# Kernel optimization log

Hardware: AMD Instinct MI355X
Metric: run time of the kernel (lower is better)

## Reference

```python
import jax, jax.numpy as jnp
import numpy as np

B, N, M, C = 8, 76725, 32, 12  # N = 9 anchors x (80^2+40^2+20^2+10^2+5^2) for a 640x640 image, P3-P7
IMG = 640.0


def setup_inputs() -> dict:
    key = jax.random.key(0)
    ks = jax.random.split(key, 7)
    # logits biased toward prior_prob~0.01 like the head's bias init
    cls_logits = jax.random.normal(ks[0], (B, N, C), jnp.float32) - 4.0
    box_deltas = 0.1 * jax.random.normal(ks[1], (B, N, 4), jnp.float32)
    # plausible anchors: random centers in image, sizes 16..256
    a_xy = jax.random.uniform(ks[2], (N, 2), jnp.float32) * IMG
    a_wh = 16.0 + jax.random.uniform(ks[3], (N, 2), jnp.float32) * 240.0
    anchors = jnp.concatenate([a_xy - 0.5 * a_wh, a_xy + 0.5 * a_wh], axis=-1)
    # padded ground truth: M boxes per image, all valid
    g_xy = jax.random.uniform(ks[4], (B, M, 2), jnp.float32) * (IMG - 96.0)
    g_wh = 16.0 + jax.random.uniform(ks[5], (B, M, 2), jnp.float32) * 80.0
    gt_boxes = jnp.concatenate([g_xy, g_xy + g_wh], axis=-1)
    gt_labels = jax.random.randint(ks[6], (B, M), 0, C)
    gt_valid = jnp.ones((B, M), dtype=bool)
    return {"cls_logits": cls_logits, "box_deltas": box_deltas, "anchors": anchors,
            "gt_boxes": gt_boxes, "gt_labels": gt_labels, "gt_valid": gt_valid}


def _box_iou(anchors, gt_boxes):
    # anchors [N,4], gt_boxes [B,M,4] -> [B,N,M]
    ax1, ay1, ax2, ay2 = (anchors[:, i] for i in range(4))
    gx1, gy1, gx2, gy2 = (gt_boxes[..., i] for i in range(4))
    iw = jnp.clip(jnp.minimum(ax2[None, :, None], gx2[:, None, :])
                  - jnp.maximum(ax1[None, :, None], gx1[:, None, :]), 0.0)
    ih = jnp.clip(jnp.minimum(ay2[None, :, None], gy2[:, None, :])
                  - jnp.maximum(ay1[None, :, None], gy1[:, None, :]), 0.0)
    inter = iw * ih
    area_a = (ax2 - ax1) * (ay2 - ay1)            # [N]
    area_g = (gx2 - gx1) * (gy2 - gy1)            # [B,M]
    union = area_a[None, :, None] + area_g[:, None, :] - inter
    return inter / union


def _encode_boxes(anchors, matched):
    aw = anchors[:, 2] - anchors[:, 0]
    ah = anchors[:, 3] - anchors[:, 1]
    acx = anchors[:, 0] + 0.5 * aw
    acy = anchors[:, 1] + 0.5 * ah
    gw = matched[..., 2] - matched[..., 0]
    gh = matched[..., 3] - matched[..., 1]
    gcx = matched[..., 0] + 0.5 * gw
    gcy = matched[..., 1] + 0.5 * gh
    return jnp.stack([(gcx - acx) / aw, (gcy - acy) / ah,
                      jnp.log(gw / aw), jnp.log(gh / ah)], axis=-1)


def reference(cls_logits, box_deltas, anchors, gt_boxes, gt_labels, gt_valid):
    # --- anchor assignment (box_iou + max over GT) ---
    ious = _box_iou(anchors, gt_boxes)                       # [B,N,M]
    ious = jnp.where(gt_valid[:, None, :], ious, -1.0)
    iou_max = ious.max(axis=-1)                              # [B,N]
    idx = ious.argmax(axis=-1)                               # [B,N]
    pos = iou_max >= 0.5
    valid = pos | (iou_max < 0.4)                            # non-ignore anchors
    matched = jnp.take_along_axis(
        gt_boxes, jnp.broadcast_to(idx[:, :, None], (B, N, 4)), axis=1)  # [B,N,4]
    mlab = jnp.take_along_axis(gt_labels, idx, axis=1)       # [B,N]
    f32 = cls_logits.dtype
    cls_t = jax.nn.one_hot(mlab, C, dtype=f32) * pos[..., None].astype(f32)
    # --- sigmoid focal loss (alpha=0.25, gamma=2), mean over non-ignored elements ---
    p = jax.nn.sigmoid(cls_logits)
    ce = -(cls_t * jax.nn.log_sigmoid(cls_logits)
           + (1.0 - cls_t) * jax.nn.log_sigmoid(-cls_logits))
    pt = cls_t * p + (1.0 - cls_t) * (1.0 - p)
    alpha_t = cls_t * 0.25 + (1.0 - cls_t) * 0.75
    focal = alpha_t * (1.0 - pt) ** 2 * ce                   # [B,N,C]
    vw = valid.astype(f32)
    cls_loss = jnp.sum(focal * vw[..., None]) / jnp.maximum(jnp.sum(vw) * C, 1.0)
    # --- smooth L1 (beta=1) on positives, mean over selected elements ---
    box_t = _encode_boxes(anchors, matched)                  # [B,N,4]
    d = jnp.abs(box_deltas - box_t)
    sl1 = jnp.where(d < 1.0, 0.5 * d * d, d - 0.5)
    pw = pos.astype(f32)
    box_loss = jnp.sum(sl1 * pw[..., None]) / jnp.maximum(jnp.sum(pw) * 4.0, 1.0)
    return cls_loss + box_loss
```

## Files before the change

### kernel.cpp

```cpp
#include <hip/hip_runtime.h>
#include <math.h>

#define NB 8
#define NA 76725
#define NM 32
#define NC 12
#define BLK 256
#define CHX 300
#define NBLOCKS (CHX * NB)
#define WPB (BLK / 64)
#define NWAVES (NBLOCKS * WPB)


__global__ __launch_bounds__(BLK, 4) void retina_main(
    const float* __restrict__ cls_logits,
    const float* __restrict__ box_deltas,
    const float* __restrict__ anchors,
    const float* __restrict__ gt_boxes,
    const int* __restrict__ gt_labels,
    char* __restrict__ ws,
    int mode, int nslots, int sstride)
{
    const int b    = blockIdx.y;
    const int tid  = threadIdx.x;
    const int n    = blockIdx.x * BLK + tid;
    const bool live = (n < NA);
    const int nc   = live ? n : (NA - 1);

    const float4 a = ((const float4*)anchors)[nc];
    const float4* clp = (const float4*)(cls_logits + ((size_t)b * NA + nc) * NC);
    const float4 c0 = clp[0], c1 = clp[1], c2 = clp[2];
    const float4 d4 = ((const float4*)box_deltas)[(size_t)b * NA + nc];

    const float area_a = (a.z - a.x) * (a.w - a.y);
    const float4* gtb = (const float4*)gt_boxes + b * NM;

    float bi[4], bS[4]; int bx[4];
    #pragma unroll
    for (int q = 0; q < 4; ++q) {
        const int m0 = q * 8;
        {
            const float4 g = gtb[m0];
            const float iw = fmaxf(fminf(a.z, g.z) - fmaxf(a.x, g.x), 0.0f);
            const float ih = fmaxf(fminf(a.w, g.w) - fmaxf(a.y, g.y), 0.0f);
            bi[q] = iw * ih;
            bS[q] = area_a + (g.z - g.x) * (g.w - g.y);
            bx[q] = m0;
        }
        #pragma unroll
        for (int mm = 1; mm < 8; ++mm) {
            const int m = m0 + mm;
            const float4 g = gtb[m];
            const float iw = fmaxf(fminf(a.z, g.z) - fmaxf(a.x, g.x), 0.0f);
            const float ih = fmaxf(fminf(a.w, g.w) - fmaxf(a.y, g.y), 0.0f);
            const float inter = iw * ih;
            const float S     = area_a + (g.z - g.x) * (g.w - g.y);
            const bool gt = inter * bS[q] > bi[q] * S;
            bi[q] = gt ? inter : bi[q];
            bS[q] = gt ? S     : bS[q];
            bx[q] = gt ? m     : bx[q];
        }
    }
    float Bi = bi[0], BS = bS[0]; int Bx = bx[0];
    #pragma unroll
    for (int q = 1; q < 4; ++q) {
        const bool gt = bi[q] * BS > Bi * bS[q];
        Bi = gt ? bi[q] : Bi;
        BS = gt ? bS[q] : BS;
        Bx = gt ? bx[q] : Bx;
    }
    const float Bu = BS - Bi;

    const bool pos   = live && (Bi >= 0.5f * Bu);
    const bool valid = live && (pos || (Bi < 0.4f * Bu));

    const float4 g  = ((const float4*)gt_boxes)[b * NM + Bx];
    const int    ml = gt_labels[b * NM + Bx];
    const int    lab = pos ? ml : -1;

    float x[NC];
    x[0]=c0.x; x[1]=c0.y; x[2]=c0.z; x[3]=c0.w;
    x[4]=c1.x; x[5]=c1.y; x[6]=c1.z; x[7]=c1.w;
    x[8]=c2.x; x[9]=c2.y; x[10]=c2.z; x[11]=c2.w;
    float facc = 0.0f;
    #pragma unroll
    for (int c = 0; c < NC; ++c) {
        const float xx = x[c];
        const bool tgt = (c == lab);
        const float z  = tgt ? -xx : xx;
        const float e  = __expf(-fabsf(xx));
        const float t  = 1.0f + e;
        const float l  = __logf(t);
        const float u  = __builtin_amdgcn_rcpf(t);
        const float v  = e * u;
        const float q  = (z >= 0.0f) ? u : v;
        const float s  = l + fmaxf(z, 0.0f);
        const float al = tgt ? 0.25f : 0.75f;
        facc += al * (q * q) * s;
    }

    float sacc = 0.0f;
    {
        const float aw  = a.z - a.x;
        const float ah  = a.w - a.y;
        const float r_aw = __builtin_amdgcn_rcpf(aw);
        const float r_ah = __builtin_amdgcn_rcpf(ah);
        const float acx = a.x + 0.5f * aw;
        const float acy = a.y + 0.5f * ah;
        const float gw  = g.z - g.x;
        const float gh  = g.w - g.y;
        const float gcx = g.x + 0.5f * gw;
        const float gcy = g.y + 0.5f * gh;
        const float t0 = (gcx - acx) * r_aw;
        const float t1 = (gcy - acy) * r_ah;
        const float t2 = __logf(gw * r_aw);
        const float t3 = __logf(gh * r_ah);
        float d;
        d = fabsf(d4.x - t0); sacc += (d < 1.0f) ? 0.5f * d * d : d - 0.5f;
        d = fabsf(d4.y - t1); sacc += (d < 1.0f) ? 0.5f * d * d : d - 0.5f;
        d = fabsf(d4.z - t2); sacc += (d < 1.0f) ? 0.5f * d * d : d - 0.5f;
        d = fabsf(d4.w - t3); sacc += (d < 1.0f) ? 0.5f * d * d : d - 0.5f;
    }

    float4 v4 = make_float4(valid ? facc : 0.0f,
                            pos   ? sacc : 0.0f,
                            valid ? 1.0f : 0.0f,
                            pos   ? 1.0f : 0.0f);
    #pragma unroll
    for (int off = 32; off > 0; off >>= 1) {
        v4.x += __shfl_down(v4.x, off);
        v4.y += __shfl_down(v4.y, off);
        v4.z += __shfl_down(v4.z, off);
        v4.w += __shfl_down(v4.w, off);
    }
    const int lane = tid & 63;
    if (lane == 0) {
        const int wid = (b * CHX + blockIdx.x) * WPB + (tid >> 6);
        if (mode == 3) {
            ((float4*)ws)[wid] = v4;
        } else {
            double* p = (double*)(ws + (size_t)(wid & (nslots - 1)) * sstride);
            atomicAdd(&p[0], (double)v4.x);
            atomicAdd(&p[1], (double)v4.y);
            atomicAdd(&p[2], (double)v4.z);
            atomicAdd(&p[3], (double)v4.w);
        }
    }
}

__global__ __launch_bounds__(1024) void retina_finalize(
    const char* __restrict__ ws, int mode, int nslots, int sstride,
    float* __restrict__ out)
{
    const int tid = threadIdx.x;
    double fs = 0.0, ss = 0.0, vc = 0.0, pc = 0.0;
    if (mode == 3) {
        const float4* sl = (const float4*)ws;
        for (int i = tid; i < nslots; i += 1024) {
            const float4 v = sl[i];
            fs += v.x; ss += v.y; vc += v.z; pc += v.w;
        }
    } else {
        for (int i = tid; i < nslots; i += 1024) {
            const double* p = (const double*)(ws + (size_t)i * sstride);
            fs += p[0]; ss += p[1]; vc += p[2]; pc += p[3];
        }
    }
    #pragma unroll
    for (int off = 32; off > 0; off >>= 1) {
        fs += __shfl_down(fs, off);
        ss += __shfl_down(ss, off);
        vc += __shfl_down(vc, off);
        pc += __shfl_down(pc, off);
    }
    __shared__ double sred[16][4];
    const int wave = tid >> 6;
    const int lane = tid & 63;
    if (lane == 0) {
        sred[wave][0] = fs; sred[wave][1] = ss;
        sred[wave][2] = vc; sred[wave][3] = pc;
    }
    __syncthreads();
    if (tid == 0) {
        #pragma unroll
        for (int w = 1; w < 16; ++w) {
            fs += sred[w][0]; ss += sred[w][1];
            vc += sred[w][2]; pc += sred[w][3];
        }
        const double cls_loss = fs / fmax(vc * (double)NC, 1.0);
        const double box_loss = ss / fmax(pc * 4.0, 1.0);
        out[0] = (float)(cls_loss + box_loss);
    }
}

extern "C" void kernel_launch(void* const* d_in, const int* in_sizes, int n_in,
                              void* d_out, int out_size, void* d_ws, size_t ws_size,
                              hipStream_t stream) {
    const float* cls_logits = (const float*)d_in[0];
    const float* box_deltas = (const float*)d_in[1];
    const float* anchors    = (const float*)d_in[2];
    const float* gt_boxes   = (const float*)d_in[3];
    const int*   gt_labels  = (const int*)d_in[4];
    float* out = (float*)d_out;

    int mode, nslots, sstride;
    if (ws_size >= (size_t)NWAVES * 16)     { mode = 3; nslots = NWAVES; sstride = 16; }
    else if (ws_size >= (size_t)(64 * 64))  { mode = 1; nslots = 64;     sstride = 64; }
    else                                    { mode = 0; nslots = 1;      sstride = 32; }

    if (mode != 3)
        hipMemsetAsync(d_ws, 0, (size_t)nslots * sstride, stream);

    dim3 grid(CHX, NB);
    retina_main<<<grid, BLK, 0, stream>>>(
        cls_logits, box_deltas, anchors, gt_boxes, gt_labels,
        (char*)d_ws, mode, nslots, sstride);
    retina_finalize<<<1, 1024, 0, stream>>>(
        (const char*)d_ws, mode, nslots, sstride, out);
}
```

Before: 107.6 us.

## Process two anchors per thread and stage GT boxes in shared memory

Each thread now handles two anchors, which halves the grid (CHX becomes about 150) and the number of per-wave partial results and atomics. GT boxes, their areas and labels are loaded once per block into shared memory with a barrier, replacing repeated global loads and per-anchor area recomputation. The launch-bounds occupancy hint drops from 4 to 3 blocks to leave room for the extra registers, which may reduce latency hiding in this memory-bound kernel.

```diff
diff --git a/kernel.cpp b/kernel.cpp
--- a/kernel.cpp
+++ b/kernel.cpp
@@ -6,13 +6,14 @@
 #define NM 32
 #define NC 12
 #define BLK 256
-#define CHX 300
+#define APB (2 * BLK)
+#define CHX ((NA + APB - 1) / APB)
 #define NBLOCKS (CHX * NB)
 #define WPB (BLK / 64)
 #define NWAVES (NBLOCKS * WPB)
 
 
-__global__ __launch_bounds__(BLK, 4) void retina_main(
+__global__ __launch_bounds__(BLK, 3) void retina_main(
     const float* __restrict__ cls_logits,
     const float* __restrict__ box_deltas,
     const float* __restrict__ anchors,
@@ -21,111 +22,132 @@
     char* __restrict__ ws,
     int mode, int nslots, int sstride)
 {
-    const int b    = blockIdx.y;
-    const int tid  = threadIdx.x;
-    const int n    = blockIdx.x * BLK + tid;
-    const bool live = (n < NA);
-    const int nc   = live ? n : (NA - 1);
-
-    const float4 a = ((const float4*)anchors)[nc];
-    const float4* clp = (const float4*)(cls_logits + ((size_t)b * NA + nc) * NC);
-    const float4 c0 = clp[0], c1 = clp[1], c2 = clp[2];
-    const float4 d4 = ((const float4*)box_deltas)[(size_t)b * NA + nc];
-
-    const float area_a = (a.z - a.x) * (a.w - a.y);
-    const float4* gtb = (const float4*)gt_boxes + b * NM;
-
-    float bi[4], bS[4]; int bx[4];
+    __shared__ float4 s_gt[NM];
+    __shared__ float  s_area[NM];
+    __shared__ int    s_lab[NM];
+
+    const int b   = blockIdx.y;
+    const int tid = threadIdx.x;
+    const int nA  = blockIdx.x * APB + tid;
+    const int nB  = nA + BLK;
+    const bool liveA = (nA < NA);
+    const bool liveB = (nB < NA);
+    const int ncA = liveA ? nA : (NA - 1);
+    const int ncB = liveB ? nB : (NA - 1);
+
+    const float4 aA = ((const float4*)anchors)[ncA];
+    const float4 aB = ((const float4*)anchors)[ncB];
+    const float4* clpA = (const float4*)(cls_logits + ((size_t)b * NA + ncA) * NC);
+    const float4* clpB = (const float4*)(cls_logits + ((size_t)b * NA + ncB) * NC);
+    const float4 cA0 = clpA[0], cA1 = clpA[1], cA2 = clpA[2];
+    const float4 cB0 = clpB[0], cB1 = clpB[1], cB2 = clpB[2];
+    const float4 dA = ((const float4*)box_deltas)[(size_t)b * NA + ncA];
+    const float4 dB = ((const float4*)box_deltas)[(size_t)b * NA + ncB];
+
+    if (tid < NM) {
+        const float4 g = ((const float4*)gt_boxes)[b * NM + tid];
+        s_gt[tid]   = g;
+        s_area[tid] = (g.z - g.x) * (g.w - g.y);
+        s_lab[tid]  = gt_labels[b * NM + tid];
+    }
+    __syncthreads();
+
+    const float areaA = (aA.z - aA.x) * (aA.w - aA.y);
+    const float areaB = (aB.z - aB.x) * (aB.w - aB.y);
+
+#define IOU_INIT(aa, ar, g, sg, m, bi, bS, bx) do {                              \
+        const float iw_ = fmaxf(fminf((aa).z, (g).z) - fmaxf((aa).x, (g).x), 0.0f); \
+        const float ih_ = fmaxf(fminf((aa).w, (g).w) - fmaxf((aa).y, (g).y), 0.0f); \
+        (bi) = iw_ * ih_; (bS) = (ar) + (sg); (bx) = (m);                        \
+    } while (0)
+#define IOU_STEP(aa, ar, g, sg, m, bi, bS, bx) do {                              \
+        const float iw_ = fmaxf(fminf((aa).z, (g).z) - fmaxf((aa).x, (g).x), 0.0f); \
+        const float ih_ = fmaxf(fminf((aa).w, (g).w) - fmaxf((aa).y, (g).y), 0.0f); \
+        const float in_ = iw_ * ih_;                                             \
+        const float S_  = (ar) + (sg);                                           \
+        const bool gt_  = in_ * (bS) > (bi) * S_;  \
+        (bi) = gt_ ? in_ : (bi); (bS) = gt_ ? S_ : (bS); (bx) = gt_ ? (m) : (bx);\
+    } while (0)
+
+    float biA[4], bSA[4], biB[4], bSB[4];
+    int   bxA[4], bxB[4];
     #pragma unroll
     for (int q = 0; q < 4; ++q) {
         const int m0 = q * 8;
         {
-            const float4 g = gtb[m0];
-            const float iw = fmaxf(fminf(a.z, g.z) - fmaxf(a.x, g.x), 0.0f);
-            const float ih = fmaxf(fminf(a.w, g.w) - fmaxf(a.y, g.y), 0.0f);
-            bi[q] = iw * ih;
-            bS[q] = area_a + (g.z - g.x) * (g.w - g.y);
-            bx[q] = m0;
+            const float4 g = s_gt[m0]; const float sg = s_area[m0];
+            IOU_INIT(aA, areaA, g, sg, m0, biA[q], bSA[q], bxA[q]);
+            IOU_INIT(aB, areaB, g, sg, m0, biB[q], bSB[q], bxB[q]);
         }
         #pragma unroll
         for (int mm = 1; mm < 8; ++mm) {
             const int m = m0 + mm;
-            const float4 g = gtb[m];
-            const float iw = fmaxf(fminf(a.z, g.z) - fmaxf(a.x, g.x), 0.0f);
-            const float ih = fmaxf(fminf(a.w, g.w) - fmaxf(a.y, g.y), 0.0f);
-            const float inter = iw * ih;
-            const float S     = area_a + (g.z - g.x) * (g.w - g.y);
-            const bool gt = inter * bS[q] > bi[q] * S;
-            bi[q] = gt ? inter : bi[q];
-            bS[q] = gt ? S     : bS[q];
-            bx[q] = gt ? m     : bx[q];
-        }
-    }
-    float Bi = bi[0], BS = bS[0]; int Bx = bx[0];
+            const float4 g = s_gt[m]; const float sg = s_area[m];
+            IOU_STEP(aA, areaA, g, sg, m, biA[q], bSA[q], bxA[q]);
+            IOU_STEP(aB, areaB, g, sg, m, biB[q], bSB[q], bxB[q]);
+        }
+    }
+    float BiA = biA[0], BSA = bSA[0]; int BxA = bxA[0];
+    float BiB = biB[0], BSB = bSB[0]; int BxB = bxB[0];
     #pragma unroll
     for (int q = 1; q < 4; ++q) {
-        const bool gt = bi[q] * BS > Bi * bS[q];
-        Bi = gt ? bi[q] : Bi;
-        BS = gt ? bS[q] : BS;
-        Bx = gt ? bx[q] : Bx;
-    }
-    const float Bu = BS - Bi;
-
-    const bool pos   = live && (Bi >= 0.5f * Bu);
-    const bool valid = live && (pos || (Bi < 0.4f * Bu));
-
-    const float4 g  = ((const float4*)gt_boxes)[b * NM + Bx];
-    const int    ml = gt_labels[b * NM + Bx];
-    const int    lab = pos ? ml : -1;
-
-    float x[NC];
-    x[0]=c0.x; x[1]=c0.y; x[2]=c0.z; x[3]=c0.w;
-    x[4]=c1.x; x[5]=c1.y; x[6]=c1.z; x[7]=c1.w;
-    x[8]=c2.x; x[9]=c2.y; x[10]=c2.z; x[11]=c2.w;
-    float facc = 0.0f;
-    #pragma unroll
-    for (int c = 0; c < NC; ++c) {
-        const float xx = x[c];
-        const bool tgt = (c == lab);
-        const float z  = tgt ? -xx : xx;
-        const float e  = __expf(-fabsf(xx));
-        const float t  = 1.0f + e;
-        const float l  = __logf(t);
-        const float u  = __builtin_amdgcn_rcpf(t);
-        const float v  = e * u;
-        const float q  = (z >= 0.0f) ? u : v;
-        const float s  = l + fmaxf(z, 0.0f);
-        const float al = tgt ? 0.25f : 0.75f;
-        facc += al * (q * q) * s;
-    }
-
-    float sacc = 0.0f;
-    {
-        const float aw  = a.z - a.x;
-        const float ah  = a.w - a.y;
-        const float r_aw = __builtin_amdgcn_rcpf(aw);
-        const float r_ah = __builtin_amdgcn_rcpf(ah);
-        const float acx = a.x + 0.5f * aw;
-        const float acy = a.y + 0.5f * ah;
-        const float gw  = g.z - g.x;
-        const float gh  = g.w - g.y;
-        const float gcx = g.x + 0.5f * gw;
-        const float gcy = g.y + 0.5f * gh;
-        const float t0 = (gcx - acx) * r_aw;
-        const float t1 = (gcy - acy) * r_ah;
-        const float t2 = __logf(gw * r_aw);
-        const float t3 = __logf(gh * r_ah);
-        float d;
-        d = fabsf(d4.x - t0); sacc += (d < 1.0f) ? 0.5f * d * d : d - 0.5f;
-        d = fabsf(d4.y - t1); sacc += (d < 1.0f) ? 0.5f * d * d : d - 0.5f;
-        d = fabsf(d4.z - t2); sacc += (d < 1.0f) ? 0.5f * d * d : d - 0.5f;
-        d = fabsf(d4.w - t3); sacc += (d < 1.0f) ? 0.5f * d * d : d - 0.5f;
-    }
-
-    float4 v4 = make_float4(valid ? facc : 0.0f,
-                            pos   ? sacc : 0.0f,
-                            valid ? 1.0f : 0.0f,
-                            pos   ? 1.0f : 0.0f);
+        bool gt = biA[q] * BSA > BiA * bSA[q];
+        BiA = gt ? biA[q] : BiA; BSA = gt ? bSA[q] : BSA; BxA = gt ? bxA[q] : BxA;
+        gt = biB[q] * BSB > BiB * bSB[q];
+        BiB = gt ? biB[q] : BiB; BSB = gt ? bSB[q] : BSB; BxB = gt ? bxB[q] : BxB;
+    }
+
+    auto epi = [&](const float4 a, const float4 c0, const float4 c1, const float4 c2,
+                   const float4 d4, const float Bi, const float BS, const int Bx,
+                   const bool live) -> float4 {
+        const float Bu = BS - Bi;
+        const bool pos   = live && (Bi >= 0.5f * Bu);
+        const bool valid = live && (pos || (Bi < 0.4f * Bu));
+        const float4 g = s_gt[Bx];
+        const int lab = pos ? s_lab[Bx] : -1;
+        float facc = 0.0f;
+#define FOCAL1(xx, cc) do {                                      \
+            const bool tgt_ = ((cc) == lab);                     \
+            const float z_ = tgt_ ? -(xx) : (xx);                \
+            const float e_ = __expf(-fabsf(xx));                 \
+            const float t_ = 1.0f + e_;               \
+            const float l_ = __logf(t_);           \
+            const float u_ = __builtin_amdgcn_rcpf(t_);          \
+            const float v_ = e_ * u_;                            \
+            const float q_ = (z_ >= 0.0f) ? u_ : v_;   \
+            const float s_ = l_ + fmaxf(z_, 0.0f);     \
+            facc += (tgt_ ? 0.25f : 0.75f) * (q_ * q_) * s_;     \
+        } while (0)
+        FOCAL1(c0.x, 0); FOCAL1(c0.y, 1); FOCAL1(c0.z,  2); FOCAL1(c0.w,  3);
+        FOCAL1(c1.x, 4); FOCAL1(c1.y, 5); FOCAL1(c1.z,  6); FOCAL1(c1.w,  7);
+        FOCAL1(c2.x, 8); FOCAL1(c2.y, 9); FOCAL1(c2.z, 10); FOCAL1(c2.w, 11);
+#undef FOCAL1
+        float sacc = 0.0f;
+        {
+            const float aw = a.z - a.x, ah = a.w - a.y;
+            const float r_aw = __builtin_amdgcn_rcpf(aw);
+            const float r_ah = __builtin_amdgcn_rcpf(ah);
+            const float acx = a.x + 0.5f * aw, acy = a.y + 0.5f * ah;
+            const float gw = g.z - g.x, gh = g.w - g.y;
+            const float gcx = g.x + 0.5f * gw, gcy = g.y + 0.5f * gh;
+            const float t0 = (gcx - acx) * r_aw;
+            const float t1 = (gcy - acy) * r_ah;
+            const float t2 = __logf(gw * r_aw);
+            const float t3 = __logf(gh * r_ah);
+            float d;
+            d = fabsf(d4.x - t0); sacc += (d < 1.0f) ? 0.5f * d * d : d - 0.5f;
+            d = fabsf(d4.y - t1); sacc += (d < 1.0f) ? 0.5f * d * d : d - 0.5f;
+            d = fabsf(d4.z - t2); sacc += (d < 1.0f) ? 0.5f * d * d : d - 0.5f;
+            d = fabsf(d4.w - t3); sacc += (d < 1.0f) ? 0.5f * d * d : d - 0.5f;
+        }
+        return make_float4(valid ? facc : 0.0f, pos ? sacc : 0.0f,
+                           valid ? 1.0f : 0.0f, pos ? 1.0f : 0.0f);
+    };
+
+    const float4 rA = epi(aA, cA0, cA1, cA2, dA, BiA, BSA, BxA, liveA);
+    const float4 rB = epi(aB, cB0, cB1, cB2, dB, BiB, BSB, BxB, liveB);
+    float4 v4 = make_float4(rA.x + rB.x, rA.y + rB.y, rA.z + rB.z, rA.w + rB.w);
+
     #pragma unroll
     for (int off = 32; off > 0; off >>= 1) {
         v4.x += __shfl_down(v4.x, off);
```

Result: slower. 126.8 us (+17.9%).
